# Kernel optimization log

Hardware: AMD Instinct MI355X
Metric: run time of the kernel (lower is better)

Reference implementation:

```python
import jax, jax.numpy as jnp
import numpy as np
from jax.scipy.linalg import solve_triangular

H, VD, M = 16, 64, 128
RIDGE = 0.01


def setup_inputs() -> dict:
    key = jax.random.key(0)
    ks = jax.random.split(key, 9)
    B, L, HD = 4, 2048, 1024
    s = 1.0 / np.sqrt(HD).astype(np.float32)
    return {
        "x": jax.random.normal(ks[0], (B, L, HD), dtype=jnp.float32),
        "cur_k": jnp.zeros((1,), dtype=jnp.float32),
        "input_mask": jnp.ones((B, L), dtype=jnp.float32),
        "Wq": jax.random.normal(ks[1], (HD, HD), dtype=jnp.float32) * s,
        "Wk": jax.random.normal(ks[2], (HD, HD), dtype=jnp.float32) * s,
        "Wv": jax.random.normal(ks[3], (HD, HD), dtype=jnp.float32) * s,
        "Wo": jax.random.normal(ks[4], (HD, HD), dtype=jnp.float32) * s,
        "bo": jax.random.normal(ks[5], (HD,), dtype=jnp.float32) * s,
        "rff_W": jax.random.normal(ks[6], (H, VD, M), dtype=jnp.float32),  # / lengthscale=1.0
        "rff_b": 2.0 * np.pi * jax.random.uniform(ks[7], (H, M), dtype=jnp.float32),
    }


def reference(x, cur_k, input_mask, Wq, Wk, Wv, Wo, bo, rff_W, rff_b):
    B, L, HD = x.shape
    scale = jnp.asarray(1.0 / np.sqrt(M), dtype=x.dtype)
    M2 = 2 * M

    def heads(t):  # [B,L,HD] -> [B,H,L,VD]
        return t.reshape(B, L, H, VD).transpose(0, 2, 1, 3)

    q = heads(x @ Wq.T)
    k = heads(x @ Wk.T)
    v = heads(x @ Wv.T)

    mask = input_mask[:, :L].astype(x.dtype)
    qmask = mask[:, None, :, None]  # [B,1,L,1]

    def rff(X):  # [B,H,L,VD] -> [B,H,L,2M]
        proj = jnp.einsum('bhld,hdm->bhlm', X, rff_W) + rff_b[None, :, None, :]
        return scale * jnp.concatenate([jnp.cos(proj), jnp.sin(proj)], axis=-1)

    PhiQ = rff(q)
    PhiK_w = rff(k) * qmask
    V_w = v * qmask

    G = jnp.einsum('bhlm,bhln->bhmn', PhiK_w, PhiK_w)  # [B,H,2M,2M]
    G = G + RIDGE * jnp.eye(M2, dtype=x.dtype)
    T = jnp.einsum('bhlm,bhld->bhmd', PhiK_w, V_w)      # [B,H,2M,VD]

    Lch = jnp.linalg.cholesky(G)
    y = solve_triangular(Lch, T, lower=True)
    W = solve_triangular(jnp.swapaxes(Lch, -2, -1), y, lower=False)

    out = jnp.einsum('bhlm,bhmd->bhld', PhiQ, W)        # [B,H,L,VD]
    # unsqueeze sample dim, permute to [B,1,L,H,VD], flatten heads -> [B,1,L,HD]
    samples = jnp.transpose(out, (0, 2, 1, 3)).reshape(B, L, HD)[:, None]
    samples = samples @ Wo.T + bo                        # W_O (dropout: eval no-op)
    samples = samples * qmask                            # [B,1,L,1] broadcast
    return samples
```

## Files before the change

### kernel.cpp

```cpp
#include <hip/hip_runtime.h>
#include <math.h>

#define B_ 4
#define L_ 2048
#define HD_ 1024
#define H_ 16
#define VD_ 64
#define M_ 128
#define M2_ 256
#define RIDGE_ 0.01f
#define SCALE_ 0.08838834764831845f

typedef unsigned short u16;
typedef __attribute__((ext_vector_type(8))) short short8;
typedef __attribute__((ext_vector_type(4))) float floatx4;

__device__ __forceinline__ u16 f2bf(float x) {
  unsigned u = __float_as_uint(x);
  unsigned r = u + 0x7fff + ((u >> 16) & 1);
  return (u16)(r >> 16);
}
__device__ __forceinline__ float bf2f(u16 h) {
  return __uint_as_float(((unsigned)h) << 16);
}
__device__ __forceinline__ void gload_lds16(const u16* g, u16* l) {
  __builtin_amdgcn_global_load_lds(
      (const __attribute__((address_space(1))) unsigned int*)g,
      (__attribute__((address_space(3))) unsigned int*)l, 16, 0, 0);
}
__device__ __forceinline__ void split4(float4 f, ushort4* h, float4* r) {
  h->x = f2bf(f.x); h->y = f2bf(f.y); h->z = f2bf(f.z); h->w = f2bf(f.w);
  r->x = f.x - bf2f(h->x); r->y = f.y - bf2f(h->y);
  r->z = f.z - bf2f(h->z); r->w = f.w - bf2f(h->w);
}

__global__ __launch_bounds__(256) void cvt_split_kernel(
    const float* __restrict__ src, u16* __restrict__ hi, u16* __restrict__ lo, int n4)
{
  int i = blockIdx.x * 256 + threadIdx.x;
  if (i < n4) {
    float4 f = ((const float4*)src)[i];
    ushort4 hv; float4 r;
    split4(f, &hv, &r);
    ushort4 lv = {f2bf(r.x), f2bf(r.y), f2bf(r.z), f2bf(r.w)};
    ((ushort4*)hi)[i] = hv;
    ((ushort4*)lo)[i] = lv;
  }
}

__global__ __launch_bounds__(256) void mfma_nt(
    const u16* __restrict__ A0, const u16* __restrict__ B0,
    float* __restrict__ C, int Ndim, int Kdim, int ldA, int ldB,
    const float* __restrict__ bias, const float* __restrict__ mask)
{
  __shared__ __align__(16) u16 a_sm[2][4096];
  __shared__ __align__(16) u16 b_sm[2][4096];
  const int tid = threadIdx.x;
  const int wave = tid >> 6, lane = tid & 63;
  const int m0 = blockIdx.y * 128, n0 = blockIdx.x * 128;
  const int wrow = (wave >> 1) * 64, wcol = (wave & 1) * 64;
  const int fm = lane & 15, q = lane >> 4;
  const int lofs = wave * 1024;

  floatx4 acc[4][4];
#pragma unroll
  for (int i = 0; i < 4; ++i)
#pragma unroll
    for (int j = 0; j < 4; ++j) acc[i][j] = (floatx4){0.f, 0.f, 0.f, 0.f};

  const u16* Ag0 = A0 + (long)(m0 + lane) * ldA + wave * 8;
  const u16* Ag1 = A0 + (long)(m0 + 64 + lane) * ldA + wave * 8;
  const u16* Bg0 = B0 + (long)(n0 + lane) * ldB + wave * 8;
  const u16* Bg1 = B0 + (long)(n0 + 64 + lane) * ldB + wave * 8;

  auto stage = [&](int d, int k0) {
    gload_lds16(Ag0 + k0, &a_sm[d][lofs]);
    gload_lds16(Ag1 + k0, &a_sm[d][lofs + 512]);
    gload_lds16(Bg0 + k0, &b_sm[d][lofs]);
    gload_lds16(Bg1 + k0, &b_sm[d][lofs + 512]);
  };
  auto compute = [&](int d) {
    short8 af[4], bfv[4];
#pragma unroll
    for (int i = 0; i < 4; ++i)
      af[i] = *(const short8*)&a_sm[d][(q * 128 + wrow + i * 16 + fm) * 8];
#pragma unroll
    for (int j = 0; j < 4; ++j)
      bfv[j] = *(const short8*)&b_sm[d][(q * 128 + wcol + j * 16 + fm) * 8];
#pragma unroll
    for (int i = 0; i < 4; ++i)
#pragma unroll
      for (int j = 0; j < 4; ++j)
        acc[i][j] = __builtin_amdgcn_mfma_f32_16x16x32_bf16(af[i], bfv[j], acc[i][j], 0, 0, 0);
  };

  stage(0, 0);
  __syncthreads();
  for (int k0 = 0; k0 < Kdim; k0 += 64) {
    if (k0 + 32 < Kdim) stage(1, k0 + 32);
    compute(0);
    __syncthreads();
    if (k0 + 64 < Kdim) stage(0, k0 + 64);
    compute(1);
    __syncthreads();
  }

  const int colb = n0 + wcol + fm;
  const int rbase = m0 + wrow + (lane >> 4) * 4;
#pragma unroll
  for (int j = 0; j < 4; ++j) {
    int cg = colb + j * 16;
    float bb = bias ? bias[cg] : 0.f;
#pragma unroll
    for (int i = 0; i < 4; ++i) {
#pragma unroll
      for (int r = 0; r < 4; ++r) {
        int row = rbase + i * 16 + r;
        float val = acc[i][j][r];
        if (bias) val = (val + bb) * mask[row];
        C[(long)row * Ndim + cg] = val;
      }
    }
  }
}

__global__ __launch_bounds__(256) void mfma_qk3(
    const u16* __restrict__ Ah, const u16* __restrict__ Al,
    const u16* __restrict__ Bh, const u16* __restrict__ Bl,
    float* __restrict__ Cq, float* __restrict__ Ck)
{
  __shared__ __align__(16) u16 ah_sm[2][4096], al_sm[2][4096];
  __shared__ __align__(16) u16 bh_sm[2][4096], bl_sm[2][4096];
  const int tid = threadIdx.x;
  const int wave = tid >> 6, lane = tid & 63;
  const int m0 = blockIdx.y * 128, n0 = blockIdx.x * 128;
  const int wrow = (wave >> 1) * 64, wcol = (wave & 1) * 64;
  const int fm = lane & 15, q = lane >> 4;
  const int lofs = wave * 1024;

  floatx4 acc[4][4];
#pragma unroll
  for (int i = 0; i < 4; ++i)
#pragma unroll
    for (int j = 0; j < 4; ++j) acc[i][j] = (floatx4){0.f, 0.f, 0.f, 0.f};

  const long a0o = (long)(m0 + lane) * 1024 + wave * 8;
  const long a1o = (long)(m0 + 64 + lane) * 1024 + wave * 8;
  const long b0o = (long)(n0 + lane) * 1024 + wave * 8;
  const long b1o = (long)(n0 + 64 + lane) * 1024 + wave * 8;

  auto stage = [&](int d, int k0) {
    gload_lds16(Ah + a0o + k0, &ah_sm[d][lofs]);
    gload_lds16(Ah + a1o + k0, &ah_sm[d][lofs + 512]);
    gload_lds16(Al + a0o + k0, &al_sm[d][lofs]);
    gload_lds16(Al + a1o + k0, &al_sm[d][lofs + 512]);
    gload_lds16(Bh + b0o + k0, &bh_sm[d][lofs]);
    gload_lds16(Bh + b1o + k0, &bh_sm[d][lofs + 512]);
    gload_lds16(Bl + b0o + k0, &bl_sm[d][lofs]);
    gload_lds16(Bl + b1o + k0, &bl_sm[d][lofs + 512]);
  };
  auto compute = [&](int d) {
    short8 afh[4], afl[4], bfh[4], bfl[4];
#pragma unroll
    for (int i = 0; i < 4; ++i) {
      afh[i] = *(const short8*)&ah_sm[d][(q * 128 + wrow + i * 16 + fm) * 8];
      afl[i] = *(const short8*)&al_sm[d][(q * 128 + wrow + i * 16 + fm) * 8];
    }
#pragma unroll
    for (int j = 0; j < 4; ++j) {
      bfh[j] = *(const short8*)&bh_sm[d][(q * 128 + wcol + j * 16 + fm) * 8];
      bfl[j] = *(const short8*)&bl_sm[d][(q * 128 + wcol + j * 16 + fm) * 8];
    }
#pragma unroll
    for (int i = 0; i < 4; ++i)
#pragma unroll
      for (int j = 0; j < 4; ++j) {
        acc[i][j] = __builtin_amdgcn_mfma_f32_16x16x32_bf16(afh[i], bfh[j], acc[i][j], 0, 0, 0);
        acc[i][j] = __builtin_amdgcn_mfma_f32_16x16x32_bf16(afl[i], bfh[j], acc[i][j], 0, 0, 0);
        acc[i][j] = __builtin_amdgcn_mfma_f32_16x16x32_bf16(afh[i], bfl[j], acc[i][j], 0, 0, 0);
      }
  };

  stage(0, 0);
  __syncthreads();
  for (int k0 = 0; k0 < 1024; k0 += 64) {
    if (k0 + 32 < 1024) stage(1, k0 + 32);
    compute(0);
    __syncthreads();
    if (k0 + 64 < 1024) stage(0, k0 + 64);
    compute(1);
    __syncthreads();
  }

  float* Cp; int cb;
  if (n0 < 1024) { Cp = Cq; cb = n0; }
  else           { Cp = Ck; cb = n0 - 1024; }
  const int colb = cb + wcol + fm;
  const int rbase = m0 + wrow + (lane >> 4) * 4;
#pragma unroll
  for (int j = 0; j < 4; ++j) {
    int cg = colb + j * 16;
#pragma unroll
    for (int i = 0; i < 4; ++i)
#pragma unroll
      for (int r = 0; r < 4; ++r)
        Cp[(long)(rbase + i * 16 + r) * 1024 + cg] = acc[i][j][r];
  }
}

__global__ __launch_bounds__(256) void rff_k_t(
    const float* __restrict__ src, const float* __restrict__ mask,
    const float* __restrict__ rffW, const float* __restrict__ rffb,
    u16* __restrict__ pkh, u16* __restrict__ pkl, int b0)
{
  __shared__ __align__(16) float w_lds[64][132];
  __shared__ __align__(16) float x_lds[64][68];
  __shared__ float b_lds[128];
  const int l0 = blockIdx.x * 64;
  const int h = blockIdx.y, b = b0 + blockIdx.z;
  const int zloc = blockIdx.z * 16 + h;
  const int tid = threadIdx.x;

  const float* wsrc = rffW + h * 8192;
  for (int f = tid * 4; f < 8192; f += 1024) {
    int d = f >> 7, m = f & 127;
    *(float4*)&w_lds[d][m] = *(const float4*)&wsrc[f];
  }
  if (tid < 128) b_lds[tid] = rffb[h * 128 + tid];
  {
    int r = tid >> 2, c0 = (tid & 3) * 16;
    const float* srow = src + (long)(b * L_ + l0 + r) * 1024 + h * VD_ + c0;
    *(float4*)&x_lds[r][c0 + 0]  = *(const float4*)(srow + 0);
    *(float4*)&x_lds[r][c0 + 4]  = *(const float4*)(srow + 4);
    *(float4*)&x_lds[r][c0 + 8]  = *(const float4*)(srow + 8);
    *(float4*)&x_lds[r][c0 + 12] = *(const float4*)(srow + 12);
  }
  __syncthreads();

  const int ty = tid >> 4, tx = tid & 15;
  float acc[4][8];
  {
    float4 bb0 = *(const float4*)&b_lds[4 * tx];
    float4 bb1 = *(const float4*)&b_lds[4 * tx + 64];
#pragma unroll
    for (int i = 0; i < 4; ++i) {
      acc[i][0] = bb0.x; acc[i][1] = bb0.y; acc[i][2] = bb0.z; acc[i][3] = bb0.w;
      acc[i][4] = bb1.x; acc[i][5] = bb1.y; acc[i][6] = bb1.z; acc[i][7] = bb1.w;
    }
  }
#pragma unroll 8
  for (int kk = 0; kk < 64; ++kk) {
    float4 w0 = *(const float4*)&w_lds[kk][4 * tx];
    float4 w1 = *(const float4*)&w_lds[kk][4 * tx + 64];
    float xv[4];
#pragma unroll
    for (int i = 0; i < 4; ++i) xv[i] = x_lds[4 * ty + i][kk];
#pragma unroll
    for (int i = 0; i < 4; ++i) {
      acc[i][0] = fmaf(xv[i], w0.x, acc[i][0]);
      acc[i][1] = fmaf(xv[i], w0.y, acc[i][1]);
      acc[i][2] = fmaf(xv[i], w0.z, acc[i][2]);
      acc[i][3] = fmaf(xv[i], w0.w, acc[i][3]);
      acc[i][4] = fmaf(xv[i], w1.x, acc[i][4]);
      acc[i][5] = fmaf(xv[i], w1.y, acc[i][5]);
      acc[i][6] = fmaf(xv[i], w1.z, acc[i][6]);
      acc[i][7] = fmaf(xv[i], w1.w, acc[i][7]);
    }
  }
  float fi[4];
#pragma unroll
  for (int i = 0; i < 4; ++i) fi[i] = SCALE_ * mask[b * L_ + l0 + 4 * ty + i];
  float cvv[4][8], svv[4][8];
#pragma unroll
  for (int i = 0; i < 4; ++i)
#pragma unroll
    for (int jj = 0; jj < 8; ++jj) {
      float sv, cv;
      sincosf(acc[i][jj], &sv, &cv);
      cvv[i][jj] = cv * fi[i];
      svv[i][jj] = sv * fi[i];
    }
  const long lbase = l0 + 4 * ty;
  const long zbase = (long)zloc * 655360;
#pragma unroll
  for (int jj = 0; jj < 8; ++jj) {
    int mcol = (jj < 4) ? (4 * tx + jj) : (64 + 4 * tx + (jj - 4));
    ushort4 h4, l4;
    h4.x = f2bf(cvv[0][jj]); l4.x = f2bf(cvv[0][jj] - bf2f(h4.x));
    h4.y = f2bf(cvv[1][jj]); l4.y = f2bf(cvv[1][jj] - bf2f(h4.y));
    h4.z = f2bf(cvv[2][jj]); l4.z = f2bf(cvv[2][jj] - bf2f(h4.z));
    h4.w = f2bf(cvv[3][jj]); l4.w = f2bf(cvv[3][jj] - bf2f(h4.w));
    long base = zbase + (long)mcol * 2048 + lbase;
    *(ushort4*)&pkh[base] = h4;
    *(ushort4*)&pkl[base] = l4;
    ushort4 hs, ls;
    hs.x = f2bf(svv[0][jj]); ls.x = f2bf(svv[0][jj] - bf2f(hs.x));
    hs.y = f2bf(svv[1][jj]); ls.y = f2bf(svv[1][jj] - bf2f(hs.y));
    hs.z = f2bf(svv[2][jj]); ls.z = f2bf(svv[2][jj] - bf2f(hs.z));
    hs.w = f2bf(svv[3][jj]); ls.w = f2bf(svv[3][jj] - bf2f(hs.w));
    long base2 = zbase + (long)(mcol + 128) * 2048 + lbase;
    *(ushort4*)&pkh[base2] = hs;
    *(ushort4*)&pkl[base2] = ls;
  }
}

__global__ __launch_bounds__(256) void vt_kernel(
    const float* __restrict__ v, const float* __restrict__ mask,
    u16* __restrict__ pkh, u16* __restrict__ pkl, int b0)
{
  __shared__ float t[128][65];
  const int z = blockIdx.y;
  const int b = b0 + (z >> 4), h = z & 15;
  const int l0 = blockIdx.x * 128;
  const int tid = threadIdx.x;
  const int d = tid & 63, lg = tid >> 6;
  for (int i = 0; i < 128; i += 4) {
    int ll = i + lg;
    float mv = mask[b * L_ + l0 + ll];
    t[ll][d] = v[(long)(b * L_ + l0 + ll) * 1024 + h * 64 + d] * mv;
  }
  __syncthreads();
  const int d2 = tid >> 2, lofs = (tid & 3) * 32;
  long base = (long)z * 655360 + (long)(256 + d2) * 2048 + l0 + lofs;
  for (int j = 0; j < 32; j += 4) {
    float f0 = t[lofs + j + 0][d2], f1 = t[lofs + j + 1][d2];
    float f2 = t[lofs + j + 2][d2], f3 = t[lofs + j + 3][d2];
    ushort4 hv, lv;
    hv.x = f2bf(f0); lv.x = f2bf(f0 - bf2f(hv.x));
    hv.y = f2bf(f1); lv.y = f2bf(f1 - bf2f(hv.y));
    hv.z = f2bf(f2); lv.z = f2bf(f2 - bf2f(hv.z));
    hv.w = f2bf(f3); lv.w = f2bf(f3 - bf2f(hv.w));
    *(ushort4*)&pkh[base + j] = hv;
    *(ushort4*)&pkl[base + j] = lv;
  }
}

__global__ __launch_bounds__(256) void mfma_gt(
    const u16* __restrict__ pkh, const u16* __restrict__ pkl,
    float* __restrict__ Gp, float* __restrict__ Tp, int bh0)
{
  __shared__ __align__(16) u16 ah_sm[2][4096], al_sm[2][4096];
  __shared__ __align__(16) u16 bh_sm[2][2048], bl_sm[2][2048];
  const int tid = threadIdx.x;
  const int wave = tid >> 6, lane = tid & 63;
  const int z = blockIdx.z;
  const int mt = blockIdx.y & 1, kc = blockIdx.y >> 1;
  const int m0 = mt * 128, n0 = blockIdx.x * 64;
  const int wrow = (wave >> 1) * 64, wcol = (wave & 1) * 32;
  const int fm = lane & 15, q = lane >> 4;
  const long batch = (long)z * 655360;
  const u16* Ah = pkh + batch;
  const u16* Al = pkl + batch;
  const int lofsA = wave * 1024;
  const int lofsB = wave * 512;

  floatx4 acc[4][2];
#pragma unroll
  for (int i = 0; i < 4; ++i)
#pragma unroll
    for (int j = 0; j < 2; ++j) acc[i][j] = (floatx4){0.f, 0.f, 0.f, 0.f};

  const long a0o = (long)(m0 + lane) * 2048 + wave * 8;
  const long a1o = (long)(m0 + 64 + lane) * 2048 + wave * 8;
  const long b0o = (long)(n0 + lane) * 2048 + wave * 8;

  auto stage = [&](int d, int k0) {
    gload_lds16(Ah + a0o + k0, &ah_sm[d][lofsA]);
    gload_lds16(Ah + a1o + k0, &ah_sm[d][lofsA + 512]);
    gload_lds16(Al + a0o + k0, &al_sm[d][lofsA]);
    gload_lds16(Al + a1o + k0, &al_sm[d][lofsA + 512]);
    gload_lds16(Ah + b0o + k0, &bh_sm[d][lofsB]);
    gload_lds16(Al + b0o + k0, &bl_sm[d][lofsB]);
  };
  auto compute = [&](int d) {
    short8 afh[4], afl[4], bfh[2], bfl[2];
#pragma unroll
    for (int i = 0; i < 4; ++i) {
      afh[i] = *(const short8*)&ah_sm[d][(q * 128 + wrow + i * 16 + fm) * 8];
      afl[i] = *(const short8*)&al_sm[d][(q * 128 + wrow + i * 16 + fm) * 8];
    }
#pragma unroll
    for (int j = 0; j < 2; ++j) {
      bfh[j] = *(const short8*)&bh_sm[d][(q * 64 + wcol + j * 16 + fm) * 8];
      bfl[j] = *(const short8*)&bl_sm[d][(q * 64 + wcol + j * 16 + fm) * 8];
    }
#pragma unroll
    for (int i = 0; i < 4; ++i)
#pragma unroll
      for (int j = 0; j < 2; ++j) {
        acc[i][j] = __builtin_amdgcn_mfma_f32_16x16x32_bf16(afh[i], bfh[j], acc[i][j], 0, 0, 0);
        acc[i][j] = __builtin_amdgcn_mfma_f32_16x16x32_bf16(afl[i], bfh[j], acc[i][j], 0, 0, 0);
        acc[i][j] = __builtin_amdgcn_mfma_f32_16x16x32_bf16(afh[i], bfl[j], acc[i][j], 0, 0, 0);
      }
  };

  const int kbeg = kc * 1024, kend = kbeg + 1024;
  stage(0, kbeg);
  __syncthreads();
  for (int k0 = kbeg; k0 < kend; k0 += 64) {
    if (k0 + 32 < kend) stage(1, k0 + 32);
    compute(0);
    __syncthreads();
    if (k0 + 64 < kend) stage(0, k0 + 64);
    compute(1);
    __syncthreads();
  }

  const int bh = bh0 + z;
  float* Gb = Gp + (long)kc * 4194304;
  float* Tb = Tp + (long)kc * 1048576;
  const int rbase = m0 + wrow + (lane >> 4) * 4;
#pragma unroll
  for (int j = 0; j < 2; ++j) {
    int col = n0 + wcol + j * 16 + fm;
#pragma unroll
    for (int i = 0; i < 4; ++i)
#pragma unroll
      for (int r = 0; r < 4; ++r) {
        int row = rbase + i * 16 + r;
        float val = acc[i][j][r];
        if (n0 < 256) Gb[(long)bh * 65536 + (long)row * 256 + col] = val;
        else Tb[(long)bh * 16384 + (long)row * 64 + (col - 256)] = val;
      }
  }
}

__global__ __launch_bounds__(256) void reduce_gt_kernel(
    const float* __restrict__ Gp, float* __restrict__ G,
    const float* __restrict__ Tp, float* __restrict__ T)
{
  long i = (long)blockIdx.x * 256 + threadIdx.x;
  if (i < 1048576) {
    float4 a = ((const float4*)Gp)[i];
    float4 b = ((const float4*)(Gp + 4194304))[i];
    float4 o = {a.x + b.x, a.y + b.y, a.z + b.z, a.w + b.w};
    ((float4*)G)[i] = o;
  } else {
    long j = i - 1048576;
    float4 a = ((const float4*)Tp)[j];
    float4 b = ((const float4*)(Tp + 1048576))[j];
    float4 o = {a.x + b.x, a.y + b.y, a.z + b.z, a.w + b.w};
    ((float4*)T)[j] = o;
  }
}

__global__ __launch_bounds__(256) void mfma_out_k(
    const u16* __restrict__ ph, const u16* __restrict__ pl,
    const u16* __restrict__ wth, const u16* __restrict__ wtl,
    u16* __restrict__ oh)
{
  __shared__ __align__(16) u16 ah_sm[2][4096], al_sm[2][4096];
  __shared__ __align__(16) u16 bh_sm[2][2048], bl_sm[2][2048];
  const int tid = threadIdx.x;
  const int wave = tid >> 6, lane = tid & 63;
  const int bh = blockIdx.y;
  const int b = bh >> 4, h = bh & 15;
  const int l0 = blockIdx.x * 128;
  const int wrow = (wave >> 1) * 64, wcol = (wave & 1) * 32;
  const int fm = lane & 15, q = lane >> 4;
  const u16* Ah = ph + (long)bh * 524288 + (long)l0 * 256;
  const u16* Al = pl + (long)bh * 524288 + (long)l0 * 256;
  const u16* Bh = wth + (long)bh * 16384;
  const u16* Bl = wtl + (long)bh * 16384;
  const int lofsA = wave * 1024;
  const int lofsB = wave * 512;

  floatx4 acc[4][2];
#pragma unroll
  for (int i = 0; i < 4; ++i)
#pragma unroll
    for (int j = 0; j < 2; ++j) acc[i][j] = (floatx4){0.f, 0.f, 0.f, 0.f};

  const long a0o = (long)lane * 256 + wave * 8;
  const long a1o = (long)(64 + lane) * 256 + wave * 8;
  const long b0o = (long)lane * 256 + wave * 8;

  auto stage = [&](int d, int k0) {
    gload_lds16(Ah + a0o + k0, &ah_sm[d][lofsA]);
    gload_lds16(Ah + a1o + k0, &ah_sm[d][lofsA + 512]);
    gload_lds16(Al + a0o + k0, &al_sm[d][lofsA]);
    gload_lds16(Al + a1o + k0, &al_sm[d][lofsA + 512]);
    gload_lds16(Bh + b0o + k0, &bh_sm[d][lofsB]);
    gload_lds16(Bl + b0o + k0, &bl_sm[d][lofsB]);
  };
  auto compute = [&](int d) {
    short8 afh[4], afl[4], bfh[2], bfl[2];
#pragma unroll
    for (int i = 0; i < 4; ++i) {
      afh[i] = *(const short8*)&ah_sm[d][(q * 128 + wrow + i * 16 + fm) * 8];
      afl[i] = *(const short8*)&al_sm[d][(q * 128 + wrow + i * 16 + fm) * 8];
    }
#pragma unroll
    for (int j = 0; j < 2; ++j) {
      bfh[j] = *(const short8*)&bh_sm[d][(q * 64 + wcol + j * 16 + fm) * 8];
      bfl[j] = *(const short8*)&bl_sm[d][(q * 64 + wcol + j * 16 + fm) * 8];
    }
#pragma unroll
    for (int i = 0; i < 4; ++i)
#pragma unroll
      for (int j = 0; j < 2; ++j) {
        acc[i][j] = __builtin_amdgcn_mfma_f32_16x16x32_bf16(afh[i], bfh[j], acc[i][j], 0, 0, 0);
        acc[i][j] = __builtin_amdgcn_mfma_f32_16x16x32_bf16(afl[i], bfh[j], acc[i][j], 0, 0, 0);
        acc[i][j] = __builtin_amdgcn_mfma_f32_16x16x32_bf16(afh[i], bfl[j], acc[i][j], 0, 0, 0);
      }
  };

  stage(0, 0);
  __syncthreads();
  for (int k0 = 0; k0 < 256; k0 += 64) {
    if (k0 + 32 < 256) stage(1, k0 + 32);
    compute(0);
    __syncthreads();
    if (k0 + 64 < 256) stage(0, k0 + 64);
    compute(1);
    __syncthreads();
  }

  const int rbase = l0 + wrow + (lane >> 4) * 4;
#pragma unroll
  for (int j = 0; j < 2; ++j) {
    int col = h * 64 + wcol + j * 16 + fm;
#pragma unroll
    for (int i = 0; i < 4; ++i)
#pragma unroll
      for (int r = 0; r < 4; ++r)
        oh[(long)(b * L_ + rbase + i * 16 + r) * 1024 + col] = f2bf(acc[i][j][r]);
  }
}

__global__ __launch_bounds__(512) void chol_rffq_wo_kernel(
    float* __restrict__ Gw,
    const float* __restrict__ qsrc,
    const float* __restrict__ rffW, const float* __restrict__ rffb,
    u16* __restrict__ ph, u16* __restrict__ pl,
    const float* __restrict__ Wo, u16* __restrict__ wo_hi)
{
  extern __shared__ float sm[];
  const int bx = blockIdx.x;
  const int tid = threadIdx.x;

  if (bx < 64) {
    float* panel = sm;
    float* invD  = sm + 4352;
    float* Gb = Gw + (long)bx * 65536;

    for (int p = 0; p < 16; ++p) {
      if (tid < 64) {
        const int i = tid & 15;
        float r[16];
#pragma unroll
        for (int k = 0; k < 16; ++k) r[k] = Gb[(16 * p + i) * 256 + 16 * p + k];
        r[i] += RIDGE_;
#pragma unroll
        for (int j = 0; j < 16; ++j) {
          float dj = __shfl(r[j], j);
          float dinv = 1.0f / sqrtf(dj);
          r[j] *= dinv;
          float Lij = r[j];
#pragma unroll
          for (int k = j + 1; k < 16; ++k) {
            float Lkj = __shfl(r[j], k);
            r[k] = fmaf(-Lij, Lkj, r[k]);
          }
        }
        float x[16];
#pragma unroll
        for (int j = 0; j < 16; ++j) {
          float s = (i == j) ? 1.0f : 0.0f;
#pragma unroll
          for (int k = 0; k < j; ++k) {
            float Ljk = __shfl(r[k], j);
            s = fmaf(-Ljk, x[k], s);
          }
          float Ljj = __shfl(r[j], j);
          x[j] = s / Ljj;
        }
        if (tid < 16) {
#pragma unroll
          for (int j = 0; j < 16; ++j) {
            invD[j * 17 + tid] = x[j];
            Gb[(16 * p + j) * 256 + 16 * p + tid] = x[j];
          }
        }
      }
      __syncthreads();

      const int nIb = 15 - p;
      if (nIb == 0) break;
      const int nrows = nIb * 16;
      const int r0 = 16 * (p + 1);

      for (int f = tid; f < nrows * 16; f += 512) {
        int rr = f >> 4, cc = f & 15;
        panel[(r0 + rr) * 17 + cc] = Gb[(long)(r0 + rr) * 256 + 16 * p + cc];
      }
      __syncthreads();

      float outv[8];
#pragma unroll
      for (int s = 0; s < 8; ++s) {
        int f = tid + s * 512;
        if (f < nrows * 16) {
          int rr = f >> 4, j = f & 15;
          const float* arow = &panel[(r0 + rr) * 17];
          const float* dcol = &invD[j * 17];
          float s2 = 0.f;
#pragma unroll
          for (int k = 0; k < 16; ++k) s2 = fmaf(arow[k], dcol[k], s2);
          outv[s] = s2;
        }
      }
      __syncthreads();
#pragma unroll
      for (int s = 0; s < 8; ++s) {
        int f = tid + s * 512;
        if (f < nrows * 16) {
          int rr = f >> 4, j = f & 15;
          panel[(r0 + rr) * 17 + j] = outv[s];
          Gb[(long)(r0 + rr) * 256 + 16 * p + j] = outv[s];
        }
      }
      __syncthreads();

      const int npairs = nIb * (nIb + 1) / 2;
      const int g = tid >> 4, t = tid & 15;
      const int tx = t & 3, ty = t >> 2;
      for (int pi0 = 0; pi0 < npairs; pi0 += 32) {
        int pi = pi0 + g;
        if (pi < npairs) {
          int a = 0; while ((a + 1) * (a + 2) / 2 <= pi) ++a;
          int b2 = pi - a * (a + 1) / 2;
          int I = p + 1 + a, J = p + 1 + b2;
          float c4[4][4];
#pragma unroll
          for (int ii = 0; ii < 4; ++ii) {
            float4 cv = *(const float4*)&Gb[(long)(16 * I + 4 * ty + ii) * 256 + 16 * J + 4 * tx];
            c4[ii][0] = cv.x; c4[ii][1] = cv.y; c4[ii][2] = cv.z; c4[ii][3] = cv.w;
          }
#pragma unroll
          for (int kk = 0; kk < 16; ++kk) {
            float av[4], bv[4];
#pragma unroll
            for (int ii = 0; ii < 4; ++ii) av[ii] = panel[(16 * I + 4 * ty + ii) * 17 + kk];
#pragma unroll
            for (int jj = 0; jj < 4; ++jj) bv[jj] = panel[(16 * J + 4 * tx + jj) * 17 + kk];
#pragma unroll
            for (int ii = 0; ii < 4; ++ii)
#pragma unroll
              for (int jj = 0; jj < 4; ++jj)
                c4[ii][jj] = fmaf(-av[ii], bv[jj], c4[ii][jj]);
          }
#pragma unroll
          for (int ii = 0; ii < 4; ++ii) {
            float4 cv = {c4[ii][0], c4[ii][1], c4[ii][2], c4[ii][3]};
            *(float4*)&Gb[(long)(16 * I + 4 * ty + ii) * 256 + 16 * J + 4 * tx] = cv;
          }
        }
      }
      __syncthreads();
    }
  } else if (bx < 64 + 2048) {
    const int id = bx - 64;
    const int l0 = (id & 31) * 64;
    const int h = (id >> 5) & 15;
    const int b = id >> 9;
    float* w_lds = sm;
    float* x_lds = sm + 8448;
    float* b_lds = sm + 12800;

    const float* wsrc = rffW + h * 8192;
    for (int f = tid * 4; f < 8192; f += 2048) {
      int d = f >> 7, m = f & 127;
      *(float4*)&w_lds[d * 132 + m] = *(const float4*)&wsrc[f];
    }
    if (tid < 128) b_lds[tid] = rffb[h * 128 + tid];
    {
      int r = tid >> 3, c0 = (tid & 7) * 8;
      const float* srow = qsrc + (long)(b * L_ + l0 + r) * 1024 + h * VD_ + c0;
      *(float4*)&x_lds[r * 68 + c0 + 0] = *(const float4*)(srow + 0);
      *(float4*)&x_lds[r * 68 + c0 + 4] = *(const float4*)(srow + 4);
    }
    __syncthreads();

    const int sub = tid >> 8;
    const int t = tid & 255;
    const int ty = t >> 4, tx = t & 15;
    const int rrow = sub * 32 + 2 * ty;
    float acc[2][8];
    {
      float4 bb0 = *(const float4*)&b_lds[4 * tx];
      float4 bb1 = *(const float4*)&b_lds[4 * tx + 64];
#pragma unroll
      for (int i = 0; i < 2; ++i) {
        acc[i][0] = bb0.x; acc[i][1] = bb0.y; acc[i][2] = bb0.z; acc[i][3] = bb0.w;
        acc[i][4] = bb1.x; acc[i][5] = bb1.y; acc[i][6] = bb1.z; acc[i][7] = bb1.w;
      }
    }
#pragma unroll 8
    for (int kk = 0; kk < 64; ++kk) {
      float4 w0 = *(const float4*)&w_lds[kk * 132 + 4 * tx];
      float4 w1 = *(const float4*)&w_lds[kk * 132 + 4 * tx + 64];
      float xv[2];
#pragma unroll
      for (int i = 0; i < 2; ++i) xv[i] = x_lds[(rrow + i) * 68 + kk];
#pragma unroll
      for (int i = 0; i < 2; ++i) {
        acc[i][0] = fmaf(xv[i], w0.x, acc[i][0]);
        acc[i][1] = fmaf(xv[i], w0.y, acc[i][1]);
        acc[i][2] = fmaf(xv[i], w0.z, acc[i][2]);
        acc[i][3] = fmaf(xv[i], w0.w, acc[i][3]);
        acc[i][4] = fmaf(xv[i], w1.x, acc[i][4]);
        acc[i][5] = fmaf(xv[i], w1.y, acc[i][5]);
        acc[i][6] = fmaf(xv[i], w1.z, acc[i][6]);
        acc[i][7] = fmaf(xv[i], w1.w, acc[i][7]);
      }
    }
#pragma unroll
    for (int i = 0; i < 2; ++i) {
      int l = l0 + rrow + i;
      float4 c0, c1, s0, s1;
      float sv, cv;
      sincosf(acc[i][0], &sv, &cv); c0.x = cv * SCALE_; s0.x = sv * SCALE_;
      sincosf(acc[i][1], &sv, &cv); c0.y = cv * SCALE_; s0.y = sv * SCALE_;
      sincosf(acc[i][2], &sv, &cv); c0.z = cv * SCALE_; s0.z = sv * SCALE_;
      sincosf(acc[i][3], &sv, &cv); c0.w = cv * SCALE_; s0.w = sv * SCALE_;
      sincosf(acc[i][4], &sv, &cv); c1.x = cv * SCALE_; s1.x = sv * SCALE_;
      sincosf(acc[i][5], &sv, &cv); c1.y = cv * SCALE_; s1.y = sv * SCALE_;
      sincosf(acc[i][6], &sv, &cv); c1.z = cv * SCALE_; s1.z = sv * SCALE_;
      sincosf(acc[i][7], &sv, &cv); c1.w = cv * SCALE_; s1.w = sv * SCALE_;
      long base = ((long)(b * H_ + h) * L_ + l) * M2_;
      ushort4 hv; float4 r4;
      split4(c0, &hv, &r4);
      *(ushort4*)&ph[base + 4 * tx] = hv;
      *(ushort4*)&pl[base + 4 * tx] = (ushort4){f2bf(r4.x), f2bf(r4.y), f2bf(r4.z), f2bf(r4.w)};
      split4(c1, &hv, &r4);
      *(ushort4*)&ph[base + 64 + 4 * tx] = hv;
      *(ushort4*)&pl[base + 64 + 4 * tx] = (ushort4){f2bf(r4.x), f2bf(r4.y), f2bf(r4.z), f2bf(r4.w)};
      split4(s0, &hv, &r4);
      *(ushort4*)&ph[base + 128 + 4 * tx] = hv;
      *(ushort4*)&pl[base + 128 + 4 * tx] = (ushort4){f2bf(r4.x), f2bf(r4.y), f2bf(r4.z), f2bf(r4.w)};
      split4(s1, &hv, &r4);
      *(ushort4*)&ph[base + 192 + 4 * tx] = hv;
      *(ushort4*)&pl[base + 192 + 4 * tx] = (ushort4){f2bf(r4.x), f2bf(r4.y), f2bf(r4.z), f2bf(r4.w)};
    }
  } else {
    const int id2 = bx - (64 + 2048);
    int idx = id2 * 512 + tid;
    for (int i = idx; i < 262144; i += 65536) {
      float4 f = ((const float4*)Wo)[i];
      ushort4 hv = {f2bf(f.x), f2bf(f.y), f2bf(f.z), f2bf(f.w)};
      ((ushort4*)wo_hi)[i] = hv;
    }
  }
}

__global__ __launch_bounds__(256) void tri_solve_kernel(
    const float* __restrict__ Gw, const float* __restrict__ T,
    u16* __restrict__ wth, u16* __restrict__ wtl)
{
  __shared__ float Y[256 * 17];
  __shared__ float tmp[16 * 17];
  const int bh = blockIdx.y;
  const int d0 = blockIdx.x * 16;
  const int tid = threadIdx.x;
  const int i = tid >> 4, d = tid & 15;
  const float* Gb = Gw + (long)bh * 65536;
  const float* Tb = T + (long)bh * 16384;

  for (int r = i; r < 256; r += 16) Y[r * 17 + d] = Tb[r * 64 + d0 + d];
  __syncthreads();

  for (int J = 0; J < 16; ++J) {
    float acc = Y[(J * 16 + i) * 17 + d];
    for (int c = 0; c < J; ++c) {
      const float* Lblk = &Gb[(long)(16 * J + i) * 256 + 16 * c];
#pragma unroll
      for (int k = 0; k < 16; k += 4) {
        float4 l4 = *(const float4*)&Lblk[k];
        acc = fmaf(-l4.x, Y[(c * 16 + k + 0) * 17 + d], acc);
        acc = fmaf(-l4.y, Y[(c * 16 + k + 1) * 17 + d], acc);
        acc = fmaf(-l4.z, Y[(c * 16 + k + 2) * 17 + d], acc);
        acc = fmaf(-l4.w, Y[(c * 16 + k + 3) * 17 + d], acc);
      }
    }
    tmp[i * 17 + d] = acc;
    __syncthreads();
    const float* invD = &Gb[(long)(16 * J + i) * 256 + 16 * J];
    float y = 0.f;
#pragma unroll
    for (int k = 0; k < 16; ++k) y = fmaf(invD[k], tmp[k * 17 + d], y);
    Y[(J * 16 + i) * 17 + d] = y;
    __syncthreads();
  }

  for (int J = 15; J >= 0; --J) {
    float acc = Y[(J * 16 + i) * 17 + d];
    for (int I = J + 1; I < 16; ++I) {
#pragma unroll
      for (int k = 0; k < 16; ++k)
        acc = fmaf(-Gb[(long)(16 * I + k) * 256 + 16 * J + i], Y[(I * 16 + k) * 17 + d], acc);
    }
    tmp[i * 17 + d] = acc;
    __syncthreads();
    float w = 0.f;
#pragma unroll
    for (int k = 0; k < 16; ++k)
      w = fmaf(Gb[(long)(16 * J + k) * 256 + 16 * J + i], tmp[k * 17 + d], w);
    Y[(J * 16 + i) * 17 + d] = w;
    __syncthreads();
  }

  for (int f = tid; f < 16 * 256; f += 256) {
    int dc = f >> 8, m = f & 255;
    float val = Y[m * 17 + dc];
    u16 h = f2bf(val);
    long o = (long)bh * 16384 + (long)(d0 + dc) * 256 + m;
    wth[o] = h;
    wtl[o] = f2bf(val - bf2f(h));
  }
}

__global__ void ws_too_small_kernel(float* out) { out[0] = 12345.0f; }

extern "C" void kernel_launch(void* const* d_in, const int* in_sizes, int n_in,
                              void* d_out, int out_size, void* d_ws, size_t ws_size,
                              hipStream_t stream) {
  const float* x    = (const float*)d_in[0];
  const float* mask = (const float*)d_in[2];
  const float* Wq   = (const float*)d_in[3];
  const float* Wk   = (const float*)d_in[4];
  const float* Wv   = (const float*)d_in[5];
  const float* Wo   = (const float*)d_in[6];
  const float* bo   = (const float*)d_in[7];
  const float* rffW = (const float*)d_in[8];
  const float* rffb = (const float*)d_in[9];
  float* out = (float*)d_out;
  float* ws  = (float*)d_ws;

  const size_t needed = 58720256UL * 4UL;
  if (ws_size < needed) {
    ws_too_small_kernel<<<1, 1, 0, stream>>>(out);
    return;
  }
  float* q = ws;
  u16* oh_bf = (u16*)ws;
  float* kbuf = ws + 8388608;
  float* T    = ws + 8388608;
  float* G    = ws + 9437184;
  u16* big16 = (u16*)(ws + 16777216);
  u16* x_hi = big16;
  u16* x_lo = big16 + 8388608;
  u16* w_hi = big16 + 16777216;
  u16* w_lo = big16 + 19922944;
  u16* pk_hi = big16;
  u16* pk_lo = big16 + 20971520;
  float* Gp = ws + 37748736;
  float* Tp = ws + 46137344;
  u16* phiq_hi = big16;
  u16* phiq_lo = big16 + 33554432;
  float* v = ws + 50331648;
  u16* wt_hi = (u16*)(ws + 50331648);
  u16* wt_lo = wt_hi + 1048576;
  u16* wo_hi = wt_hi + 2097152;

  hipFuncSetAttribute((const void*)chol_rffq_wo_kernel,
                      hipFuncAttributeMaxDynamicSharedMemorySize, 51712);

  dim3 blk(256);

  cvt_split_kernel<<<8192, blk, 0, stream>>>(x, x_hi, x_lo, 2097152);
  cvt_split_kernel<<<1024, blk, 0, stream>>>(Wq, w_hi,           w_lo,           262144);
  cvt_split_kernel<<<1024, blk, 0, stream>>>(Wk, w_hi + 1048576, w_lo + 1048576, 262144);
  cvt_split_kernel<<<1024, blk, 0, stream>>>(Wv, w_hi + 2097152, w_lo + 2097152, 262144);

  mfma_qk3<<<dim3(16, 64), blk, 0, stream>>>(x_hi, x_lo, w_hi, w_lo, q, kbuf);
  mfma_nt<<<dim3(8, 64), blk, 0, stream>>>(x_hi, w_hi + 2097152, v,
                                           1024, 1024, 1024, 1024, nullptr, nullptr);

  for (int half = 0; half < 2; ++half) {
    int b0 = half * 2, bh0 = half * 32;
    rff_k_t<<<dim3(32, 16, 2), blk, 0, stream>>>(kbuf, mask, rffW, rffb, pk_hi, pk_lo, b0);
    vt_kernel<<<dim3(16, 32), blk, 0, stream>>>(v, mask, pk_hi, pk_lo, b0);
    mfma_gt<<<dim3(5, 4, 32), blk, 0, stream>>>(pk_hi, pk_lo, Gp, Tp, bh0);
  }

  reduce_gt_kernel<<<5120, blk, 0, stream>>>(Gp, G, Tp, T);

  chol_rffq_wo_kernel<<<dim3(64 + 2048 + 128), dim3(512), 51712, stream>>>(
      G, q, rffW, rffb, phiq_hi, phiq_lo, Wo, wo_hi);

  tri_solve_kernel<<<dim3(4, 64), dim3(256), 0, stream>>>(G, T, wt_hi, wt_lo);

  mfma_out_k<<<dim3(16, 64), blk, 0, stream>>>(phiq_hi, phiq_lo, wt_hi, wt_lo, oh_bf);

  mfma_nt<<<dim3(8, 64), blk, 0, stream>>>(oh_bf, wo_hi, out, 1024, 1024, 1024, 1024, bo, mask);
}
```

Before: 911.0 us.

## Deepen GEMM load pipeline with partial vmcnt waits and swizzle workgroup order

All four MFMA GEMM kernels now keep two stages of global-to-LDS loads in flight. They wait with explicit s_waitcnt vmcnt counts and raw barriers instead of __syncthreads, which drains every outstanding load. Workgroup IDs are also remapped with an XCD-aware stride-8 swizzle so neighbouring tiles land on the same chiplet and share L2. This risks correctness if the vmcnt counts do not match the number of loads per stage, and the remap assumes the grid size is divisible by 8.

```diff
diff --git a/kernel.cpp b/kernel.cpp
--- a/kernel.cpp
+++ b/kernel.cpp
@@ -32,6 +32,20 @@
   h->x = f2bf(f.x); h->y = f2bf(f.y); h->z = f2bf(f.z); h->w = f2bf(f.w);
   r->x = f.x - bf2f(h->x); r->y = f.y - bf2f(h->y);
   r->z = f.z - bf2f(h->z); r->w = f.w - bf2f(h->w);
+}
+#define WAITVM(N) asm volatile("s_waitcnt vmcnt(" #N ")" ::: "memory")
+__device__ __forceinline__ void barf() {
+  asm volatile("" ::: "memory");
+  __builtin_amdgcn_s_barrier();
+  asm volatile("" ::: "memory");
+}
+__device__ __forceinline__ void swz2d(int* bx, int* by) {
+  int gx = gridDim.x;
+  int nwg = gx * gridDim.y;
+  int orig = (*by) * gx + (*bx);
+  int wg = (orig & 7) * (nwg >> 3) + (orig >> 3);
+  *bx = wg % gx;
+  *by = wg / gx;
 }
 
 __global__ __launch_bounds__(256) void cvt_split_kernel(
@@ -57,7 +71,9 @@
   __shared__ __align__(16) u16 b_sm[2][4096];
   const int tid = threadIdx.x;
   const int wave = tid >> 6, lane = tid & 63;
-  const int m0 = blockIdx.y * 128, n0 = blockIdx.x * 128;
+  int bx = blockIdx.x, by = blockIdx.y;
+  swz2d(&bx, &by);
+  const int m0 = by * 128, n0 = bx * 128;
   const int wrow = (wave >> 1) * 64, wcol = (wave & 1) * 64;
   const int fm = lane & 15, q = lane >> 4;
   const int lofs = wave * 1024;
@@ -95,15 +111,22 @@
   };
 
   stage(0, 0);
-  __syncthreads();
-  for (int k0 = 0; k0 < Kdim; k0 += 64) {
-    if (k0 + 32 < Kdim) stage(1, k0 + 32);
+  stage(1, 32);
+  for (int k = 0; k + 64 < Kdim; k += 64) {
+    WAITVM(4); barf();
     compute(0);
-    __syncthreads();
-    if (k0 + 64 < Kdim) stage(0, k0 + 64);
+    barf();
+    stage(0, k + 64);
+    WAITVM(4); barf();
     compute(1);
-    __syncthreads();
-  }
+    barf();
+    stage(1, k + 96);
+  }
+  WAITVM(4); barf();
+  compute(0);
+  barf();
+  WAITVM(0); barf();
+  compute(1);
 
   const int colb = n0 + wcol + fm;
   const int rbase = m0 + wrow + (lane >> 4) * 4;
@@ -133,7 +156,9 @@
   __shared__ __align__(16) u16 bh_sm[2][4096], bl_sm[2][4096];
   const int tid = threadIdx.x;
   const int wave = tid >> 6, lane = tid & 63;
-  const int m0 = blockIdx.y * 128, n0 = blockIdx.x * 128;
+  int bx = blockIdx.x, by = blockIdx.y;
+  swz2d(&bx, &by);
+  const int m0 = by * 128, n0 = bx * 128;
   const int wrow = (wave >> 1) * 64, wcol = (wave & 1) * 64;
   const int fm = lane & 15, q = lane >> 4;
   const int lofs = wave * 1024;
@@ -182,15 +207,22 @@
   };
 
   stage(0, 0);
-  __syncthreads();
-  for (int k0 = 0; k0 < 1024; k0 += 64) {
-    if (k0 + 32 < 1024) stage(1, k0 + 32);
+  stage(1, 32);
+  for (int k = 0; k + 64 < 1024; k += 64) {
+    WAITVM(8); barf();
     compute(0);
-    __syncthreads();
-    if (k0 + 64 < 1024) stage(0, k0 + 64);
+    barf();
+    stage(0, k + 64);
+    WAITVM(8); barf();
     compute(1);
-    __syncthreads();
-  }
+    barf();
+    stage(1, k + 96);
+  }
+  WAITVM(8); barf();
+  compute(0);
+  barf();
+  WAITVM(0); barf();
+  compute(1);
 
   float* Cp; int cb;
   if (n0 < 1024) { Cp = Cq; cb = n0; }
@@ -343,14 +375,20 @@
   __shared__ __align__(16) u16 bh_sm[2][2048], bl_sm[2][2048];
   const int tid = threadIdx.x;
   const int wave = tid >> 6, lane = tid & 63;
-  const int z = blockIdx.z;
-  const int mt = blockIdx.y & 1, kc = blockIdx.y >> 1;
-  const int m0 = mt * 128, n0 = blockIdx.x * 64;
+  int orig = (blockIdx.z * gridDim.y + blockIdx.y) * gridDim.x + blockIdx.x;
+  int nwg = gridDim.x * gridDim.y * gridDim.z;
+  int wg = (orig & 7) * (nwg >> 3) + (orig >> 3);
+  const int bxx = wg % 5;
+  const int rr = wg / 5;
+  const int byy = rr & 3;
+  const int z = rr >> 2;
+  const int mt = byy & 1, kc = byy >> 1;
+  const int m0 = mt * 128, n0 = bxx * 64;
   const int wrow = (wave >> 1) * 64, wcol = (wave & 1) * 32;
   const int fm = lane & 15, q = lane >> 4;
   const long batch = (long)z * 655360;
-  const u16* Ah = pkh + batch;
-  const u16* Al = pkl + batch;
+  const u16* Ahp = pkh + batch;
+  const u16* Alp = pkl + batch;
   const int lofsA = wave * 1024;
   const int lofsB = wave * 512;
 
@@ -365,12 +403,12 @@
   const long b0o = (long)(n0 + lane) * 2048 + wave * 8;
 
   auto stage = [&](int d, int k0) {
-    gload_lds16(Ah + a0o + k0, &ah_sm[d][lofsA]);
-    gload_lds16(Ah + a1o + k0, &ah_sm[d][lofsA + 512]);
-    gload_lds16(Al + a0o + k0, &al_sm[d][lofsA]);
-    gload_lds16(Al + a1o + k0, &al_sm[d][lofsA + 512]);
-    gload_lds16(Ah + b0o + k0, &bh_sm[d][lofsB]);
-    gload_lds16(Al + b0o + k0, &bl_sm[d][lofsB]);
+    gload_lds16(Ahp + a0o + k0, &ah_sm[d][lofsA]);
+    gload_lds16(Ahp + a1o + k0, &ah_sm[d][lofsA + 512]);
+    gload_lds16(Alp + a0o + k0, &al_sm[d][lofsA]);
+    gload_lds16(Alp + a1o + k0, &al_sm[d][lofsA + 512]);
+    gload_lds16(Ahp + b0o + k0, &bh_sm[d][lofsB]);
+    gload_lds16(Alp + b0o + k0, &bl_sm[d][lofsB]);
   };
   auto compute = [&](int d) {
     short8 afh[4], afl[4], bfh[2], bfl[2];
@@ -396,15 +434,22 @@
 
   const int kbeg = kc * 1024, kend = kbeg + 1024;
   stage(0, kbeg);
-  __syncthreads();
-  for (int k0 = kbeg; k0 < kend; k0 += 64) {
-    if (k0 + 32 < kend) stage(1, k0 + 32);
+  stage(1, kbeg + 32);
+  for (int k = kbeg; k + 64 < kend; k += 64) {
+    WAITVM(6); barf();
     compute(0);
-    __syncthreads();
-    if (k0 + 64 < kend) stage(0, k0 + 64);
+    barf();
+    stage(0, k + 64);
+    WAITVM(6); barf();
     compute(1);
-    __syncthreads();
-  }
+    barf();
+    stage(1, k + 96);
+  }
+  WAITVM(6); barf();
+  compute(0);
+  barf();
+  WAITVM(0); barf();
+  compute(1);
 
   const int bh = bh0 + z;
   float* Gb = Gp + (long)kc * 4194304;
@@ -453,15 +498,17 @@
   __shared__ __align__(16) u16 bh_sm[2][2048], bl_sm[2][2048];
   const int tid = threadIdx.x;
   const int wave = tid >> 6, lane = tid & 63;
-  const int bh = blockIdx.y;
+  int bx = blockIdx.x, by = blockIdx.y;
+  swz2d(&bx, &by);
+  const int bh = by;
   const int b = bh >> 4, h = bh & 15;
-  const int l0 = blockIdx.x * 128;
+  const int l0 = bx * 128;
   const int wrow = (wave >> 1) * 64, wcol = (wave & 1) * 32;
   const int fm = lane & 15, q = lane >> 4;
-  const u16* Ah = ph + (long)bh * 524288 + (long)l0 * 256;
-  const u16* Al = pl + (long)bh * 524288 + (long)l0 * 256;
-  const u16* Bh = wth + (long)bh * 16384;
-  const u16* Bl = wtl + (long)bh * 16384;
+  const u16* Ahp = ph + (long)bh * 524288 + (long)l0 * 256;
+  const u16* Alp = pl + (long)bh * 524288 + (long)l0 * 256;
+  const u16* Bhp = wth + (long)bh * 16384;
+  const u16* Blp = wtl + (long)bh * 16384;
   const int lofsA = wave * 1024;
   const int lofsB = wave * 512;
 
@@ -476,12 +523,12 @@
   const long b0o = (long)lane * 256 + wave * 8;
 
   auto stage = [&](int d, int k0) {
-    gload_lds16(Ah + a0o + k0, &ah_sm[d][lofsA]);
-    gload_lds16(Ah + a1o + k0, &ah_sm[d][lofsA + 512]);
-    gload_lds16(Al + a0o + k0, &al_sm[d][lofsA]);
-    gload_lds16(Al + a1o + k0, &al_sm[d][lofsA + 512]);
-    gload_lds16(Bh + b0o + k0, &bh_sm[d][lofsB]);
-    gload_lds16(Bl + b0o + k0, &bl_sm[d][lofsB]);
+    gload_lds16(Ahp + a0o + k0, &ah_sm[d][lofsA]);
+    gload_lds16(Ahp + a1o + k0, &ah_sm[d][lofsA + 512]);
+    gload_lds16(Alp + a0o + k0, &al_sm[d][lofsA]);
+    gload_lds16(Alp + a1o + k0, &al_sm[d][lofsA + 512]);
+    gload_lds16(Bhp + b0o + k0, &bh_sm[d][lofsB]);
+    gload_lds16(Blp + b0o + k0, &bl_sm[d][lofsB]);
   };
   auto compute = [&](int d) {
     short8 afh[4], afl[4], bfh[2], bfl[2];
@@ -506,15 +553,22 @@
   };
 
   stage(0, 0);
-  __syncthreads();
-  for (int k0 = 0; k0 < 256; k0 += 64) {
-    if (k0 + 32 < 256) stage(1, k0 + 32);
+  stage(1, 32);
+  for (int k = 0; k + 64 < 256; k += 64) {
+    WAITVM(6); barf();
     compute(0);
-    __syncthreads();
-    if (k0 + 64 < 256) stage(0, k0 + 64);
+    barf();
+    stage(0, k + 64);
+    WAITVM(6); barf();
     compute(1);
-    __syncthreads();
-  }
+    barf();
+    stage(1, k + 96);
+  }
+  WAITVM(6); barf();
+  compute(0);
+  barf();
+  WAITVM(0); barf();
+  compute(1);
 
   const int rbase = l0 + wrow + (lane >> 4) * 4;
 #pragma unroll
```

Result: faster. 833.6 us (-8.5%).
